# Performance work log

Hardware: AMD Instinct MI355X
Metric: run time of the kernel (lower is better)

## Reference

```python
import jax, jax.numpy as jnp
import numpy as np

FEATURES = 4
HIDDEN = 32


def setup_inputs() -> dict:
    key = jax.random.key(0)
    ks = jax.random.split(key, 12)
    n_nodes, n_edges = 100000, 2500000
    x = jax.random.normal(ks[0], (n_nodes, FEATURES), dtype=jnp.float32)
    edge_index = jax.random.randint(ks[1], (2, n_edges), 0, n_nodes, dtype=jnp.int64)
    def glorot(k, fan_in, fan_out):
        s = jnp.sqrt(6.0 / (fan_in + fan_out)).astype(jnp.float32)
        return jax.random.uniform(k, (fan_in, fan_out), jnp.float32, -s, s)
    return {
        "x": x,
        "edge_index": edge_index,
        "W1": glorot(ks[2], FEATURES, HIDDEN), "b1": jnp.zeros((HIDDEN,), jnp.float32),
        "W2": glorot(ks[3], HIDDEN, HIDDEN),   "b2": jnp.zeros((HIDDEN,), jnp.float32),
        "W21": glorot(ks[4], HIDDEN, HIDDEN),  "b21": jnp.zeros((HIDDEN,), jnp.float32),
        "W3": glorot(ks[5], HIDDEN, 1),        "b3": jnp.zeros((1,), jnp.float32),
    }


def _gcn_norm(edge_index, n_nodes):
    # Add self-loops, compute symmetric normalization deg^-1/2[dst]*deg^-1/2[src]
    loops = jnp.arange(n_nodes, dtype=edge_index.dtype)
    src = jnp.concatenate([edge_index[0], loops])
    dst = jnp.concatenate([edge_index[1], loops])
    deg = jax.ops.segment_sum(jnp.ones_like(dst, dtype=jnp.float32), dst, num_segments=n_nodes)
    dinv = jnp.where(deg > 0, jax.lax.rsqrt(deg), 0.0)
    norm = dinv[src] * dinv[dst]  # [E+N]
    return src, dst, norm


def _gcn_layer(x, W, b, src, dst, norm, n_nodes):
    h = x @ W                                   # [N, out]
    msg = h[src] * norm[:, None]                # gather + scale
    out = jax.ops.segment_sum(msg, dst, num_segments=n_nodes)  # scatter-add
    return out + b


def reference(x, edge_index, W1, b1, W2, b2, W21, b21, W3, b3):
    n_nodes = x.shape[0]
    src, dst, norm = _gcn_norm(edge_index, n_nodes)
    h = jax.nn.relu(_gcn_layer(x, W1, b1, src, dst, norm, n_nodes))
    h = jax.nn.relu(_gcn_layer(h, W2, b2, src, dst, norm, n_nodes))
    h = jax.nn.relu(_gcn_layer(h, W21, b21, src, dst, norm, n_nodes))
    return _gcn_layer(h, W3, b3, src, dst, norm, n_nodes)
```

## Files before the change

### kernel.cpp

```cpp
#include <hip/hip_runtime.h>

#define FEATS 4
#define HID 32
#define BLK 256
#define CAP 64
#define PW 256
#define PSHIFT 8
#define PCAP 8192
#define NPB 512
#define PBLK 1024
#define MAXK 8
#define MAXNP 512

static inline int cdiv(long long a, int b) { return (int)((a + b - 1) / b); }

__global__ void k_zero_i(int* __restrict__ p, int n) {
    int i = blockIdx.x * blockDim.x + threadIdx.x;
    if (i < n) p[i] = 0;
}

__global__ void k_partition(const int* __restrict__ src, const int* __restrict__ dst,
                            int* __restrict__ part_fill, unsigned int* __restrict__ part_edges,
                            int e, int np) {
    __shared__ int lcnt[MAXNP];
    __shared__ int lbase[MAXNP];
    for (int p = threadIdx.x; p < np; p += blockDim.x) lcnt[p] = 0;
    __syncthreads();
    int chunk = (e + gridDim.x - 1) / gridDim.x;
    int lo = blockIdx.x * chunk;
    int hi = min(lo + chunk, e);
    unsigned pw[MAXK];
    int pp[MAXK];
#pragma unroll
    for (int k = 0; k < MAXK; k++) {
        int j = lo + threadIdx.x + k * (int)blockDim.x;
        if (j < hi) {
            int d = dst[j], s = src[j];
            int p = d >> PSHIFT;
            pp[k] = p;
            pw[k] = (unsigned)s | ((unsigned)(d & (PW - 1)) << 24);
            atomicAdd(&lcnt[p], 1);
        } else pp[k] = -1;
    }
    __syncthreads();
    for (int p = threadIdx.x; p < np; p += blockDim.x) {
        int c = lcnt[p];
        lbase[p] = c ? atomicAdd(&part_fill[p], c) : 0;
        lcnt[p] = 0;
    }
    __syncthreads();
#pragma unroll
    for (int k = 0; k < MAXK; k++) {
        if (pp[k] >= 0) {
            int p = pp[k];
            int pos = lbase[p] + atomicAdd(&lcnt[p], 1);
            if (pos < PCAP) part_edges[(size_t)p * PCAP + pos] = pw[k];
        }
    }
}

__global__ void k_local_csr(const int* __restrict__ part_fill,
                            const unsigned int* __restrict__ part_edges,
                            int* __restrict__ cnt_g, float* __restrict__ dinv,
                            int* __restrict__ bucket, int n) {
    __shared__ int cnt[PW];
    int p = blockIdx.x;
    if (threadIdx.x < PW) cnt[threadIdx.x] = 0;
    __syncthreads();
    int m = min(part_fill[p], PCAP);
    const unsigned int* pe = part_edges + (size_t)p * PCAP;
    int base_node = p << PSHIFT;
    for (int j = threadIdx.x; j < m; j += blockDim.x) {
        unsigned v = pe[j];
        int local = (int)(v >> 24);
        int s = (int)(v & 0xFFFFFFu);
        int pos = atomicAdd(&cnt[local], 1);
        if (pos < CAP) bucket[(size_t)(base_node + local) * CAP + pos] = s;
    }
    __syncthreads();
    if (threadIdx.x < PW) {
        int node = base_node + threadIdx.x;
        if (node < n) {
            int dg = cnt[threadIdx.x];
            cnt_g[node] = dg;
            dinv[node] = rsqrtf((float)(dg + 1));
        }
    }
}

__global__ void k_dinv(const int* __restrict__ deg, float* __restrict__ dinv, int n) {
    int i = blockIdx.x * blockDim.x + threadIdx.x;
    if (i < n) dinv[i] = rsqrtf((float)(deg[i] + 1));
}

__global__ void k_xn(const float4* __restrict__ x, const float* __restrict__ dinv,
                     float4* __restrict__ xn, int n) {
    int i = blockIdx.x * blockDim.x + threadIdx.x;
    if (i < n) {
        float4 v = x[i];
        float s = dinv[i];
        v.x *= s; v.y *= s; v.z *= s; v.w *= s;
        xn[i] = v;
    }
}

__global__ void k_gather4(const int* __restrict__ cnt, const int* __restrict__ bucket,
                          const float4* __restrict__ xn, const float* __restrict__ dinv,
                          float4* __restrict__ agg, int n) {
    int gid = blockIdx.x * blockDim.x + threadIdx.x;
    int node = gid >> 3;
    int lane = gid & 7;
    if (node >= n) return;
    int dg = min(cnt[node], CAP);
    const int* row = bucket + (size_t)node * CAP;
    float4 acc = make_float4(0.f, 0.f, 0.f, 0.f);
    int j = lane;
    for (; j + 8 < dg; j += 16) {
        int s0 = row[j], s1 = row[j + 8];
        float4 v0 = xn[s0];
        float4 v1 = xn[s1];
        acc.x += v0.x + v1.x; acc.y += v0.y + v1.y;
        acc.z += v0.z + v1.z; acc.w += v0.w + v1.w;
    }
    if (j < dg) {
        float4 v = xn[row[j]];
        acc.x += v.x; acc.y += v.y; acc.z += v.z; acc.w += v.w;
    }
#pragma unroll
    for (int o = 4; o > 0; o >>= 1) {
        acc.x += __shfl_down(acc.x, o, 8);
        acc.y += __shfl_down(acc.y, o, 8);
        acc.z += __shfl_down(acc.z, o, 8);
        acc.w += __shfl_down(acc.w, o, 8);
    }
    if (lane == 0) {
        float4 self = xn[node];
        float sc = dinv[node];
        float4 r;
        r.x = sc * (acc.x + self.x);
        r.y = sc * (acc.y + self.y);
        r.z = sc * (acc.z + self.z);
        r.w = sc * (acc.w + self.w);
        agg[node] = r;
    }
}

__global__ void k_fuse12(const float4* __restrict__ agg4,
                         const float* __restrict__ W1, const float* __restrict__ b1,
                         const float* __restrict__ W2, const float* __restrict__ dinv,
                         float* __restrict__ hn, int n) {
    __shared__ float4 sW1[FEATS * 8];
    __shared__ float4 sB1[8];
    __shared__ float4 sW2[HID * 8];
    int tid = threadIdx.x;
    if (tid < FEATS * 8) sW1[tid] = ((const float4*)W1)[tid];
    if (tid < 8) sB1[tid] = ((const float4*)b1)[tid];
    for (int i = tid; i < HID * 8; i += blockDim.x) sW2[i] = ((const float4*)W2)[i];
    __syncthreads();
    int node = blockIdx.x * blockDim.x + tid;
    if (node >= n) return;
    float4 a = agg4[node];
    float4 y4[8];
#pragma unroll
    for (int k4 = 0; k4 < 8; k4++) {
        float4 r = sB1[k4];
        float4 w0 = sW1[0 * 8 + k4], w1 = sW1[1 * 8 + k4];
        float4 w2 = sW1[2 * 8 + k4], w3 = sW1[3 * 8 + k4];
        r.x += a.x * w0.x + a.y * w1.x + a.z * w2.x + a.w * w3.x;
        r.y += a.x * w0.y + a.y * w1.y + a.z * w2.y + a.w * w3.y;
        r.z += a.x * w0.z + a.y * w1.z + a.z * w2.z + a.w * w3.z;
        r.w += a.x * w0.w + a.y * w1.w + a.z * w2.w + a.w * w3.w;
        r.x = fmaxf(r.x, 0.f); r.y = fmaxf(r.y, 0.f);
        r.z = fmaxf(r.z, 0.f); r.w = fmaxf(r.w, 0.f);
        y4[k4] = r;
    }
    float4 acc[8];
#pragma unroll
    for (int c4 = 0; c4 < 8; c4++) acc[c4] = make_float4(0.f, 0.f, 0.f, 0.f);
#pragma unroll
    for (int k4 = 0; k4 < 8; k4++) {
        float4 yv = y4[k4];
#pragma unroll
        for (int c4 = 0; c4 < 8; c4++) {
            float4 wa = sW2[(4 * k4 + 0) * 8 + c4];
            float4 wb = sW2[(4 * k4 + 1) * 8 + c4];
            float4 wc = sW2[(4 * k4 + 2) * 8 + c4];
            float4 wd = sW2[(4 * k4 + 3) * 8 + c4];
            acc[c4].x += yv.x * wa.x + yv.y * wb.x + yv.z * wc.x + yv.w * wd.x;
            acc[c4].y += yv.x * wa.y + yv.y * wb.y + yv.z * wc.y + yv.w * wd.y;
            acc[c4].z += yv.x * wa.z + yv.y * wb.z + yv.z * wc.z + yv.w * wd.z;
            acc[c4].w += yv.x * wa.w + yv.y * wb.w + yv.z * wc.w + yv.w * wd.w;
        }
    }
    float sc = dinv[node];
    float4* op = (float4*)hn + (size_t)node * 8;
#pragma unroll
    for (int c4 = 0; c4 < 8; c4++) {
        float4 r = acc[c4];
        r.x *= sc; r.y *= sc; r.z *= sc; r.w *= sc;
        op[c4] = r;
    }
}

template <int K, int C>
__global__ void k_mm(const float* __restrict__ in, const float* __restrict__ W,
                     const float* __restrict__ dinv, float* __restrict__ hn, int n) {
    __shared__ float sW[K * C];
    for (int i = threadIdx.x; i < K * C; i += blockDim.x) sW[i] = W[i];
    __syncthreads();
    int gid = blockIdx.x * blockDim.x + threadIdx.x;
    int node = gid / C, c = gid % C;
    if (node >= n) return;
    float acc = 0.0f;
#pragma unroll
    for (int k = 0; k < K; k++) acc += in[node * K + k] * sW[k * C + c];
    hn[node * C + c] = acc * dinv[node];
}

#define ACC4(v) do { acc.x += (v).x; acc.y += (v).y; acc.z += (v).z; acc.w += (v).w; } while (0)

#define GATHER_BODY()                                                        \
    int dg = min(cnt[node], CAP);                                            \
    const float4* hp = (const float4*)hn;                                    \
    const int* row = bucket + (size_t)node * CAP;                            \
    float4 acc = hp[node * 8 + cq];                                          \
    int j = 0;                                                               \
    for (; j + 8 <= dg; j += 8) {                                            \
        int4 sa = *(const int4*)(row + j);                                   \
        int4 sb = *(const int4*)(row + j + 4);                               \
        float4 v0 = hp[sa.x * 8 + cq];                                       \
        float4 v1 = hp[sa.y * 8 + cq];                                       \
        float4 v2 = hp[sa.z * 8 + cq];                                       \
        float4 v3 = hp[sa.w * 8 + cq];                                       \
        float4 v4 = hp[sb.x * 8 + cq];                                       \
        float4 v5 = hp[sb.y * 8 + cq];                                       \
        float4 v6 = hp[sb.z * 8 + cq];                                       \
        float4 v7 = hp[sb.w * 8 + cq];                                       \
        ACC4(v0); ACC4(v1); ACC4(v2); ACC4(v3);                              \
        ACC4(v4); ACC4(v5); ACC4(v6); ACC4(v7);                              \
    }                                                                        \
    if (j + 4 <= dg) {                                                       \
        int4 s4 = *(const int4*)(row + j);                                   \
        float4 v0 = hp[s4.x * 8 + cq];                                       \
        float4 v1 = hp[s4.y * 8 + cq];                                       \
        float4 v2 = hp[s4.z * 8 + cq];                                       \
        float4 v3 = hp[s4.w * 8 + cq];                                       \
        ACC4(v0); ACC4(v1); ACC4(v2); ACC4(v3);                              \
        j += 4;                                                              \
    }                                                                        \
    for (; j < dg; j++) {                                                    \
        float4 v = hp[row[j] * 8 + cq];                                      \
        ACC4(v);                                                             \
    }

__global__ void k_gather_fmm(const int* __restrict__ cnt, const int* __restrict__ bucket,
                             const float* __restrict__ hn, const float* __restrict__ dinv,
                             const float* __restrict__ bias, const float* __restrict__ Wn,
                             float* __restrict__ hn3, int n) {
    __shared__ float4 sW[HID * 8];
    sW[threadIdx.x] = ((const float4*)Wn)[threadIdx.x];
    __syncthreads();
    int gid = blockIdx.x * blockDim.x + threadIdx.x;
    int node = gid >> 3;
    int cq = gid & 7;
    if (node >= n) return;
    GATHER_BODY()
    float sc = dinv[node];
    float4 b = ((const float4*)bias)[cq];
    float4 y;
    y.x = fmaxf(sc * acc.x + b.x, 0.f);
    y.y = fmaxf(sc * acc.y + b.y, 0.f);
    y.z = fmaxf(sc * acc.z + b.z, 0.f);
    y.w = fmaxf(sc * acc.w + b.w, 0.f);
    float4 o = make_float4(0.f, 0.f, 0.f, 0.f);
#pragma unroll
    for (int r = 0; r < 8; r++) {
        float4 v;
        v.x = __shfl(y.x, r, 8);
        v.y = __shfl(y.y, r, 8);
        v.z = __shfl(y.z, r, 8);
        v.w = __shfl(y.w, r, 8);
        float4 w0 = sW[(4 * r + 0) * 8 + cq];
        float4 w1 = sW[(4 * r + 1) * 8 + cq];
        float4 w2 = sW[(4 * r + 2) * 8 + cq];
        float4 w3 = sW[(4 * r + 3) * 8 + cq];
        o.x += v.x * w0.x + v.y * w1.x + v.z * w2.x + v.w * w3.x;
        o.y += v.x * w0.y + v.y * w1.y + v.z * w2.y + v.w * w3.y;
        o.z += v.x * w0.z + v.y * w1.z + v.z * w2.z + v.w * w3.z;
        o.w += v.x * w0.w + v.y * w1.w + v.z * w2.w + v.w * w3.w;
    }
    o.x *= sc; o.y *= sc; o.z *= sc; o.w *= sc;
    ((float4*)hn3)[node * 8 + cq] = o;
}

__global__ void k_gather_fdot(const int* __restrict__ cnt, const int* __restrict__ bucket,
                              const float* __restrict__ hn, const float* __restrict__ dinv,
                              const float* __restrict__ bias, const float* __restrict__ W3,
                              float* __restrict__ hn4, int n) {
    int gid = blockIdx.x * blockDim.x + threadIdx.x;
    int node = gid >> 3;
    int cq = gid & 7;
    if (node >= n) return;
    GATHER_BODY()
    float sc = dinv[node];
    float4 b = ((const float4*)bias)[cq];
    float4 w = ((const float4*)W3)[cq];
    float p = fmaxf(sc * acc.x + b.x, 0.f) * w.x
            + fmaxf(sc * acc.y + b.y, 0.f) * w.y
            + fmaxf(sc * acc.z + b.z, 0.f) * w.z
            + fmaxf(sc * acc.w + b.w, 0.f) * w.w;
#pragma unroll
    for (int o = 4; o > 0; o >>= 1) p += __shfl_down(p, o, 8);
    if (cq == 0) hn4[node] = p * sc;
}

__global__ void k_gather1b(const int* __restrict__ cnt, const int* __restrict__ bucket,
                           const float* __restrict__ hn, const float* __restrict__ dinv,
                           const float* __restrict__ b, float* __restrict__ out, int n) {
    int gid = blockIdx.x * blockDim.x + threadIdx.x;
    int node = gid >> 3;
    int lane = gid & 7;
    if (node >= n) return;
    int dg = min(cnt[node], CAP);
    const int* row = bucket + (size_t)node * CAP;
    float acc = (lane == 0) ? hn[node] : 0.0f;
    int j = lane;
    for (; j + 8 < dg; j += 16) {
        float a0 = hn[row[j]];
        float a1 = hn[row[j + 8]];
        acc += a0 + a1;
    }
    if (j < dg) acc += hn[row[j]];
#pragma unroll
    for (int o = 4; o > 0; o >>= 1) acc += __shfl_down(acc, o, 8);
    if (lane == 0) out[node] = dinv[node] * acc + b[0];
}

__global__ void k_deg_count(const int* __restrict__ dst, int* __restrict__ deg, int e) {
    int i = blockIdx.x * blockDim.x + threadIdx.x;
    if (i < e) atomicAdd(&deg[dst[i]], 1);
}

__global__ void k_block_scan(const int* __restrict__ deg, int* __restrict__ exc,
                             int* __restrict__ blk_sums, int n) {
    __shared__ int s[BLK];
    int i = blockIdx.x * BLK + threadIdx.x;
    int v = (i < n) ? deg[i] : 0;
    s[threadIdx.x] = v;
    __syncthreads();
    for (int off = 1; off < BLK; off <<= 1) {
        int t = (threadIdx.x >= (unsigned)off) ? s[threadIdx.x - off] : 0;
        __syncthreads();
        s[threadIdx.x] += t;
        __syncthreads();
    }
    if (i < n) exc[i] = s[threadIdx.x] - v;
    if (threadIdx.x == BLK - 1) blk_sums[blockIdx.x] = s[threadIdx.x];
}

__global__ void k_scan_sums(int* __restrict__ blk_sums, int nb) {
    __shared__ int s[1024];
    __shared__ int carry;
    if (threadIdx.x == 0) carry = 0;
    __syncthreads();
    for (int base = 0; base < nb; base += 1024) {
        int i = base + threadIdx.x;
        int v = (i < nb) ? blk_sums[i] : 0;
        s[threadIdx.x] = v;
        __syncthreads();
        for (int off = 1; off < 1024; off <<= 1) {
            int t = (threadIdx.x >= (unsigned)off) ? s[threadIdx.x - off] : 0;
            __syncthreads();
            s[threadIdx.x] += t;
            __syncthreads();
        }
        if (i < nb) blk_sums[i] = s[threadIdx.x] - v + carry;
        __syncthreads();
        if (threadIdx.x == 0) carry += s[1023];
        __syncthreads();
    }
}

__global__ void k_add_off(const int* __restrict__ exc, const int* __restrict__ blk_sums,
                          int* __restrict__ row_start, int* __restrict__ fill, int n) {
    int i = blockIdx.x * blockDim.x + threadIdx.x;
    if (i < n) {
        int rs = exc[i] + blk_sums[i / BLK];
        row_start[i] = rs;
        fill[i] = rs;
    }
}

__global__ void k_scatter(const int* __restrict__ src, const int* __restrict__ dst,
                          int* __restrict__ fill, int* __restrict__ csr_src, int e) {
    int i = blockIdx.x * blockDim.x + threadIdx.x;
    if (i < e) {
        int pos = atomicAdd(&fill[dst[i]], 1);
        csr_src[pos] = src[i];
    }
}

template <bool RELU>
__global__ void k_gather32(const int* __restrict__ row_start, const int* __restrict__ deg,
                           const int* __restrict__ csr_src, const float* __restrict__ hn,
                           const float* __restrict__ dinv, const float* __restrict__ bias,
                           float* __restrict__ y, int n) {
    int gid = blockIdx.x * blockDim.x + threadIdx.x;
    int node = gid >> 3;
    int cq = gid & 7;
    if (node >= n) return;
    int rs = row_start[node], dg = deg[node];
    const float4* hp = (const float4*)hn;
    float4 acc = hp[node * 8 + cq];
    for (int j = 0; j < dg; j++) {
        int s = csr_src[rs + j];
        float4 v = hp[s * 8 + cq];
        ACC4(v);
    }
    float sc = dinv[node];
    float4 b = ((const float4*)bias)[cq];
    float4 r;
    r.x = sc * acc.x + b.x; r.y = sc * acc.y + b.y;
    r.z = sc * acc.z + b.z; r.w = sc * acc.w + b.w;
    if (RELU) {
        r.x = fmaxf(r.x, 0.0f); r.y = fmaxf(r.y, 0.0f);
        r.z = fmaxf(r.z, 0.0f); r.w = fmaxf(r.w, 0.0f);
    }
    ((float4*)y)[node * 8 + cq] = r;
}

__global__ void k_gather1(const int* __restrict__ row_start, const int* __restrict__ deg,
                          const int* __restrict__ csr_src, const float* __restrict__ hn,
                          const float* __restrict__ dinv, const float* __restrict__ b,
                          float* __restrict__ out, int n) {
    int gid = blockIdx.x * blockDim.x + threadIdx.x;
    int node = gid >> 3;
    int lane = gid & 7;
    if (node >= n) return;
    int rs = row_start[node], dg = deg[node];
    float acc = (lane == 0) ? hn[node] : 0.0f;
    for (int j = lane; j < dg; j += 8) acc += hn[csr_src[rs + j]];
#pragma unroll
    for (int o = 4; o > 0; o >>= 1) acc += __shfl_down(acc, o, 8);
    if (lane == 0) out[node] = dinv[node] * acc + b[0];
}

extern "C" void kernel_launch(void* const* d_in, const int* in_sizes, int n_in,
                              void* d_out, int out_size, void* d_ws, size_t ws_size,
                              hipStream_t stream) {
    const float* x   = (const float*)d_in[0];
    const int*   ei  = (const int*)d_in[1];
    const float* W1  = (const float*)d_in[2];
    const float* b1  = (const float*)d_in[3];
    const float* W2  = (const float*)d_in[4];
    const float* b2  = (const float*)d_in[5];
    const float* W21 = (const float*)d_in[6];
    const float* b21 = (const float*)d_in[7];
    const float* W3  = (const float*)d_in[8];
    const float* b3  = (const float*)d_in[9];
    float* out = (float*)d_out;

    const int n = in_sizes[0] / FEATS;
    const int e = in_sizes[1] / 2;
    const int* src = ei;
    const int* dst = ei + e;
    const int nb = cdiv(n, BLK);
    const int np = cdiv(n, PW);

    auto align256 = [](size_t v) { return (v + 255) & ~(size_t)255; };
    const long long n8 = (long long)n * 8;

    size_t sz_cnt    = align256((size_t)n * 4);
    size_t sz_dinv   = align256((size_t)n * 4);
    size_t sz_f4     = align256((size_t)n * 16);
    size_t sz_bucket = align256((size_t)n * CAP * 4);
    size_t sz_hn     = align256((size_t)n * HID * 4);
    size_t sz_part   = align256((size_t)np * PCAP * 4) + align256((size_t)np * 4);
    size_t region    = 2 * sz_hn > sz_part ? 2 * sz_hn : sz_part;
    size_t need = sz_cnt + sz_dinv + 2 * sz_f4 + sz_bucket + region;

    if (ws_size >= need && np <= MAXNP && (long long)e <= (long long)NPB * PBLK * MAXK) {
        char* ws = (char*)d_ws;
        size_t off = 0;
        int*    cnt_g  = (int*)(ws + off);    off += sz_cnt;
        float*  dinv   = (float*)(ws + off);  off += sz_dinv;
        float4* xn     = (float4*)(ws + off); off += sz_f4;
        float4* agg4   = (float4*)(ws + off); off += sz_f4;
        int*    bucket = (int*)(ws + off);    off += sz_bucket;
        char*   reg    = ws + off;
        float* hn = (float*)reg;
        float* yb = (float*)(reg + sz_hn);
        unsigned int* part_edges = (unsigned int*)reg;
        int* part_fill = (int*)(reg + align256((size_t)np * PCAP * 4));

        k_zero_i<<<cdiv(np, BLK), BLK, 0, stream>>>(part_fill, np);
        k_partition<<<NPB, PBLK, 0, stream>>>(src, dst, part_fill, part_edges, e, np);
        k_local_csr<<<np, PBLK, 0, stream>>>(part_fill, part_edges, cnt_g, dinv, bucket, n);

        k_xn<<<nb, BLK, 0, stream>>>((const float4*)x, dinv, xn, n);
        k_gather4<<<cdiv(n8, BLK), BLK, 0, stream>>>(cnt_g, bucket, xn, dinv, agg4, n);
        k_fuse12<<<nb, BLK, 0, stream>>>(agg4, W1, b1, W2, dinv, hn, n);

        k_gather_fmm<<<cdiv(n8, BLK), BLK, 0, stream>>>(cnt_g, bucket, hn, dinv, b2, W21, yb, n);

        k_gather_fdot<<<cdiv(n8, BLK), BLK, 0, stream>>>(cnt_g, bucket, yb, dinv, b21, W3, hn, n);

        k_gather1b<<<cdiv(n8, BLK), BLK, 0, stream>>>(cnt_g, bucket, hn, dinv, b3, out, n);
    } else {
        const long long nc = (long long)n * HID;
        char* ws = (char*)d_ws;
        size_t off = 0;
        int*   deg_i     = (int*)(ws + off);   off += align256((size_t)n * 4);
        int*   exc       = (int*)(ws + off);   off += align256((size_t)n * 4);
        int*   row_start = (int*)(ws + off);   off += align256((size_t)n * 4);
        int*   fill      = (int*)(ws + off);   off += align256((size_t)n * 4);
        int*   blk_sums  = (int*)(ws + off);   off += align256((size_t)nb * 4);
        float* dinv      = (float*)(ws + off); off += align256((size_t)n * 4);
        int*   csr_src   = (int*)(ws + off);   off += align256((size_t)e * 4);
        float* hn        = (float*)(ws + off); off += align256((size_t)n * HID * 4);
        float* yb        = (float*)(ws + off); off += align256((size_t)n * HID * 4);

        k_zero_i<<<nb, BLK, 0, stream>>>(deg_i, n);
        k_deg_count<<<cdiv(e, BLK), BLK, 0, stream>>>(dst, deg_i, e);
        k_dinv<<<nb, BLK, 0, stream>>>(deg_i, dinv, n);
        k_block_scan<<<nb, BLK, 0, stream>>>(deg_i, exc, blk_sums, n);
        k_scan_sums<<<1, 1024, 0, stream>>>(blk_sums, nb);
        k_add_off<<<nb, BLK, 0, stream>>>(exc, blk_sums, row_start, fill, n);
        k_scatter<<<cdiv(e, BLK), BLK, 0, stream>>>(src, dst, fill, csr_src, e);

        k_mm<FEATS, HID><<<cdiv(nc, BLK), BLK, 0, stream>>>(x, W1, dinv, hn, n);
        k_gather32<true><<<cdiv(n8, BLK), BLK, 0, stream>>>(row_start, deg_i, csr_src, hn, dinv, b1, yb, n);

        k_mm<HID, HID><<<cdiv(nc, BLK), BLK, 0, stream>>>(yb, W2, dinv, hn, n);
        k_gather32<true><<<cdiv(n8, BLK), BLK, 0, stream>>>(row_start, deg_i, csr_src, hn, dinv, b2, yb, n);

        k_mm<HID, HID><<<cdiv(nc, BLK), BLK, 0, stream>>>(yb, W21, dinv, hn, n);
        k_gather32<true><<<cdiv(n8, BLK), BLK, 0, stream>>>(row_start, deg_i, csr_src, hn, dinv, b21, yb, n);

        k_mm<HID, 1><<<cdiv(n, BLK), BLK, 0, stream>>>(yb, W3, dinv, hn, n);
        k_gather1<<<cdiv(n8, BLK), BLK, 0, stream>>>(row_start, deg_i, csr_src, hn, dinv, b3, out, n);
    }
}
```

Baseline: 250.4 us.

## Build CSR buckets via per-block partition runs with spill path

Replaces the global-atomic partition step with per-block, per-partition fixed-capacity runs kept in shared-memory counters, so no global atomics are needed on partition fill counters. A second kernel per partition reads all blocks' runs into local buckets, and a small spill kernel handles any overflow through global atomics. The dinv computation is folded into the x-normalisation kernel. This adds a large runs buffer and a sparse read pattern in the CSR kernel: it scans NPB*RCAP slots per partition, and most of those slots are empty.

```diff
diff --git a/kernel.cpp b/kernel.cpp
--- a/kernel.cpp
+++ b/kernel.cpp
@@ -11,12 +11,97 @@
 #define PBLK 1024
 #define MAXK 8
 #define MAXNP 512
+#define RCAP 32
+#define RSHIFT 5
+#define SPILLCAP 65536
 
 static inline int cdiv(long long a, int b) { return (int)((a + b - 1) / b); }
 
 __global__ void k_zero_i(int* __restrict__ p, int n) {
     int i = blockIdx.x * blockDim.x + threadIdx.x;
     if (i < n) p[i] = 0;
+}
+
+__global__ void k_part1(const int* __restrict__ src, const int* __restrict__ dst,
+                        unsigned int* __restrict__ runs, int* __restrict__ cnt_runs,
+                        int* __restrict__ spill_cnt, int* __restrict__ spill_d,
+                        int* __restrict__ spill_s, int e, int np) {
+    __shared__ int lcnt[MAXNP];
+    for (int p = threadIdx.x; p < np; p += blockDim.x) lcnt[p] = 0;
+    __syncthreads();
+    int chunk = (e + gridDim.x - 1) / gridDim.x;
+    int lo = blockIdx.x * chunk;
+    int hi = min(lo + chunk, e);
+    size_t rbase = (size_t)blockIdx.x * np;
+    for (int j = lo + threadIdx.x; j < hi; j += blockDim.x) {
+        int d = dst[j], s = src[j];
+        int p = d >> PSHIFT;
+        int pos = atomicAdd(&lcnt[p], 1);
+        if (pos < RCAP) {
+            runs[(rbase + p) * RCAP + pos] =
+                (unsigned)s | ((unsigned)(d & (PW - 1)) << 24);
+        } else {
+            int k = atomicAdd(spill_cnt, 1);
+            if (k < SPILLCAP) { spill_d[k] = d; spill_s[k] = s; }
+        }
+    }
+    __syncthreads();
+    for (int p = threadIdx.x; p < np; p += blockDim.x)
+        cnt_runs[rbase + p] = lcnt[p];
+}
+
+__global__ void k_csr1(const unsigned int* __restrict__ runs,
+                       const int* __restrict__ cnt_runs,
+                       int* __restrict__ cnt_g, int* __restrict__ bucket, int n, int np) {
+    __shared__ int cnt[PW];
+    __shared__ int scnt[NPB];
+    int p = blockIdx.x;
+    if (threadIdx.x < PW) cnt[threadIdx.x] = 0;
+    for (int b = threadIdx.x; b < NPB; b += blockDim.x)
+        scnt[b] = min(cnt_runs[(size_t)b * np + p], RCAP);
+    __syncthreads();
+    int base_node = p << PSHIFT;
+    for (int s = threadIdx.x; s < NPB * RCAP; s += blockDim.x) {
+        int b = s >> RSHIFT;
+        int idx = s & (RCAP - 1);
+        if (idx < scnt[b]) {
+            unsigned v = runs[((size_t)b * np + p) * RCAP + idx];
+            int local = (int)(v >> 24);
+            int sv = (int)(v & 0xFFFFFFu);
+            int pos = atomicAdd(&cnt[local], 1);
+            if (pos < CAP) bucket[(size_t)(base_node + local) * CAP + pos] = sv;
+        }
+    }
+    __syncthreads();
+    if (threadIdx.x < PW) {
+        int node = base_node + threadIdx.x;
+        if (node < n) cnt_g[node] = cnt[threadIdx.x];
+    }
+}
+
+__global__ void k_spill(const int* __restrict__ spill_cnt, const int* __restrict__ spill_d,
+                        const int* __restrict__ spill_s, int* __restrict__ cnt_g,
+                        int* __restrict__ bucket) {
+    int m = min(*spill_cnt, SPILLCAP);
+    int gid = blockIdx.x * blockDim.x + threadIdx.x;
+    int gs = gridDim.x * blockDim.x;
+    for (int i = gid; i < m; i += gs) {
+        int d = spill_d[i], s = spill_s[i];
+        int pos = atomicAdd(&cnt_g[d], 1);
+        if (pos < CAP) bucket[(size_t)d * CAP + pos] = s;
+    }
+}
+
+__global__ void k_xn(const float4* __restrict__ x, const int* __restrict__ cnt_g,
+                     float* __restrict__ dinv, float4* __restrict__ xn, int n) {
+    int i = blockIdx.x * blockDim.x + threadIdx.x;
+    if (i < n) {
+        float s = rsqrtf((float)(cnt_g[i] + 1));
+        dinv[i] = s;
+        float4 v = x[i];
+        v.x *= s; v.y *= s; v.z *= s; v.w *= s;
+        xn[i] = v;
+    }
 }
 
 __global__ void k_partition(const int* __restrict__ src, const int* __restrict__ dst,
@@ -88,13 +173,8 @@
     }
 }
 
-__global__ void k_dinv(const int* __restrict__ deg, float* __restrict__ dinv, int n) {
-    int i = blockIdx.x * blockDim.x + threadIdx.x;
-    if (i < n) dinv[i] = rsqrtf((float)(deg[i] + 1));
-}
-
-__global__ void k_xn(const float4* __restrict__ x, const float* __restrict__ dinv,
-                     float4* __restrict__ xn, int n) {
+__global__ void k_xn0(const float4* __restrict__ x, const float* __restrict__ dinv,
+                      float4* __restrict__ xn, int n) {
     int i = blockIdx.x * blockDim.x + threadIdx.x;
     if (i < n) {
         float4 v = x[i];
@@ -102,6 +182,11 @@
         v.x *= s; v.y *= s; v.z *= s; v.w *= s;
         xn[i] = v;
     }
+}
+
+__global__ void k_dinv(const int* __restrict__ deg, float* __restrict__ dinv, int n) {
+    int i = blockIdx.x * blockDim.x + threadIdx.x;
+    if (i < n) dinv[i] = rsqrtf((float)(deg[i] + 1));
 }
 
 __global__ void k_gather4(const int* __restrict__ cnt, const int* __restrict__ bucket,
@@ -475,11 +560,50 @@
     size_t sz_f4     = align256((size_t)n * 16);
     size_t sz_bucket = align256((size_t)n * CAP * 4);
     size_t sz_hn     = align256((size_t)n * HID * 4);
-    size_t sz_part   = align256((size_t)np * PCAP * 4) + align256((size_t)np * 4);
-    size_t region    = 2 * sz_hn > sz_part ? 2 * sz_hn : sz_part;
-    size_t need = sz_cnt + sz_dinv + 2 * sz_f4 + sz_bucket + region;
-
-    if (ws_size >= need && np <= MAXNP && (long long)e <= (long long)NPB * PBLK * MAXK) {
+
+    size_t sz_runs   = align256((size_t)NPB * np * RCAP * 4);
+    size_t sz_cruns  = align256((size_t)NPB * np * 4);
+    size_t sz_spill  = align256((size_t)SPILLCAP * 4);
+    size_t poolA     = 2 * sz_f4 + 2 * sz_hn;
+    if (sz_runs > poolA) poolA = sz_runs;
+    size_t needA = sz_cnt + sz_dinv + sz_cruns + 256 + 2 * sz_spill + sz_bucket + poolA;
+
+    size_t sz_part = align256((size_t)np * PCAP * 4) + align256((size_t)np * 4);
+    size_t regionB = 2 * sz_hn > sz_part ? 2 * sz_hn : sz_part;
+    size_t needB = sz_cnt + sz_dinv + 2 * sz_f4 + sz_bucket + regionB;
+
+    if (ws_size >= needA && np <= MAXNP) {
+        char* ws = (char*)d_ws;
+        size_t off = 0;
+        int*    cnt_g     = (int*)(ws + off);   off += sz_cnt;
+        float*  dinv      = (float*)(ws + off); off += sz_dinv;
+        int*    cnt_runs  = (int*)(ws + off);   off += sz_cruns;
+        int*    spill_cnt = (int*)(ws + off);   off += 256;
+        int*    spill_d   = (int*)(ws + off);   off += sz_spill;
+        int*    spill_s   = (int*)(ws + off);   off += sz_spill;
+        int*    bucket    = (int*)(ws + off);   off += sz_bucket;
+        char*   pool      = ws + off;
+        unsigned int* runs = (unsigned int*)pool;
+        float4* xn   = (float4*)pool;
+        float4* agg4 = (float4*)(pool + sz_f4);
+        float*  hn   = (float*)(pool + 2 * sz_f4);
+        float*  yb   = (float*)(pool + 2 * sz_f4 + sz_hn);
+
+        k_zero_i<<<1, 64, 0, stream>>>(spill_cnt, 1);
+        k_part1<<<NPB, PBLK, 0, stream>>>(src, dst, runs, cnt_runs,
+                                          spill_cnt, spill_d, spill_s, e, np);
+        k_csr1<<<np, PBLK, 0, stream>>>(runs, cnt_runs, cnt_g, bucket, n, np);
+        k_spill<<<16, 256, 0, stream>>>(spill_cnt, spill_d, spill_s, cnt_g, bucket);
+
+        k_xn<<<nb, BLK, 0, stream>>>((const float4*)x, cnt_g, dinv, xn, n);
+        k_gather4<<<cdiv(n8, BLK), BLK, 0, stream>>>(cnt_g, bucket, xn, dinv, agg4, n);
+        k_fuse12<<<nb, BLK, 0, stream>>>(agg4, W1, b1, W2, dinv, hn, n);
+
+        k_gather_fmm<<<cdiv(n8, BLK), BLK, 0, stream>>>(cnt_g, bucket, hn, dinv, b2, W21, yb, n);
+        k_gather_fdot<<<cdiv(n8, BLK), BLK, 0, stream>>>(cnt_g, bucket, yb, dinv, b21, W3, hn, n);
+        k_gather1b<<<cdiv(n8, BLK), BLK, 0, stream>>>(cnt_g, bucket, hn, dinv, b3, out, n);
+    } else if (ws_size >= needB && np <= MAXNP &&
+               (long long)e <= (long long)NPB * PBLK * MAXK) {
         char* ws = (char*)d_ws;
         size_t off = 0;
         int*    cnt_g  = (int*)(ws + off);    off += sz_cnt;
@@ -497,14 +621,11 @@
         k_partition<<<NPB, PBLK, 0, stream>>>(src, dst, part_fill, part_edges, e, np);
         k_local_csr<<<np, PBLK, 0, stream>>>(part_fill, part_edges, cnt_g, dinv, bucket, n);
 
-        k_xn<<<nb, BLK, 0, stream>>>((const float4*)x, dinv, xn, n);
+        k_xn0<<<nb, BLK, 0, stream>>>((const float4*)x, dinv, xn, n);
         k_gather4<<<cdiv(n8, BLK), BLK, 0, stream>>>(cnt_g, bucket, xn, dinv, agg4, n);
         k_fuse12<<<nb, BLK, 0, stream>>>(agg4, W1, b1, W2, dinv, hn, n);
-
         k_gather_fmm<<<cdiv(n8, BLK), BLK, 0, stream>>>(cnt_g, bucket, hn, dinv, b2, W21, yb, n);
-
         k_gather_fdot<<<cdiv(n8, BLK), BLK, 0, stream>>>(cnt_g, bucket, yb, dinv, b21, W3, hn, n);
-
         k_gather1b<<<cdiv(n8, BLK), BLK, 0, stream>>>(cnt_g, bucket, hn, dinv, b3, out, n);
     } else {
         const long long nc = (long long)n * HID;
```

After: 256.4 us. 2.4% more time.
